# Kernel tuning notes

Hardware: AMD Instinct MI355X
Metric: run time of the kernel (lower is better)

Reference implementation:

```python
import jax, jax.numpy as jnp
import numpy as np

COMMITMENT_COST = 0.25
CODEBOOK_SIZE = 8192
EMBED_DIM = 256


def setup_inputs() -> dict:
    key = jax.random.key(0)
    k1, k2 = jax.random.split(key)
    z = jax.random.normal(k1, (16, 256, 32, 32), dtype=jnp.float32)
    # Embedding init: uniform(-1/K, 1/K)
    emb = jax.random.uniform(k2, (CODEBOOK_SIZE, EMBED_DIM), dtype=jnp.float32,
                             minval=-1.0 / CODEBOOK_SIZE, maxval=1.0 / CODEBOOK_SIZE)
    return {"z": z, "embedding": emb}


def reference(z, embedding):
    # z: [b, c, h, w] -> [b, h, w, c]
    z = jnp.transpose(z.astype(jnp.float32), (0, 2, 3, 1))
    b, h, w, c = z.shape
    zf = z.reshape(-1, c)  # [N, c]
    # Squared distances: ||z||^2 + ||e||^2 - 2 z e^T   -> [N, K]
    d = (jnp.sum(zf * zf, axis=1, keepdims=True)
         + jnp.sum(embedding * embedding, axis=1)
         - 2.0 * jnp.einsum('nd,kd->nk', zf, embedding))
    ids = jnp.argmin(d, axis=1)  # [N] int
    z_q = embedding[ids].reshape(b, h, w, c)
    commitment_loss = COMMITMENT_COST * jnp.mean((jax.lax.stop_gradient(z_q) - z) ** 2)
    codebook_loss = jnp.mean((z_q - jax.lax.stop_gradient(z)) ** 2)
    loss = commitment_loss + codebook_loss
    # straight-through estimator
    z_q_st = z + jax.lax.stop_gradient(z_q - z)
    z_q_out = jnp.transpose(z_q_st, (0, 3, 1, 2))  # [b, c, h, w]
    return (z_q_out, loss, commitment_loss, codebook_loss, ids)
```

## Files before the change

kernel.cpp:

```cpp
#include <hip/hip_runtime.h>

#define BB    16
#define CC    256
#define HWD   1024
#define NN    16384
#define KK    8192
#define DD    256
#define ZQ_N  4194304

#define WS_ROWBEST 0
#define WS_LOSS    131072
#define WS_NEEDED  131080

#define ZB_OFF      0
#define EB_OFF      2097152
#define Q_OFF       3145728
#define SEGCNT_OFF  4192256
#define BC_OFF      4194304
#define SEGCAP      8176u
#define LQCAP       3072

#define CMARGIN  4e-4f

typedef short short8 __attribute__((ext_vector_type(8)));
typedef float f32x4  __attribute__((ext_vector_type(4)));
typedef unsigned short u16;
typedef unsigned int   u32;

static __device__ __forceinline__ u32 cenc(float x) {
    u32 u = __float_as_uint(x);
    return (u & 0x80000000u) ? ~u : (u | 0x80000000u);
}
static __device__ __forceinline__ float cdec(u32 k) {
    u32 u = (k & 0x80000000u) ? (k ^ 0x80000000u) : ~k;
    return __uint_as_float(u);
}
static __device__ __forceinline__ u16 f2bf(float f) {
    u32 u = __float_as_uint(f);
    return (u16)((u + 0x7FFFu + ((u >> 16) & 1u)) >> 16);
}

__global__ __launch_bounds__(256)
void k_prep(const float* __restrict__ z, const float* __restrict__ emb,
            u16* __restrict__ zb, u16* __restrict__ eb,
            unsigned long long* __restrict__ rowBest, double* __restrict__ lossSum,
            u32* __restrict__ bestC, u32* __restrict__ segCnt) {
    __shared__ float tile[64][65];
    const int bid = blockIdx.x;
    const int t = threadIdx.x;
    if (bid < 1024) {
        const int b = bid >> 6, d0 = ((bid >> 4) & 3) * 64, h0 = (bid & 15) * 64;
        const float* zp = z + ((size_t)b * CC + d0) * HWD + h0;
#pragma unroll
        for (int i = 0; i < 4; ++i) {
            int fid = i * 256 + t;
            int dd = fid >> 4, hq = (fid & 15) * 4;
            float4 v = *(const float4*)(zp + (size_t)dd * HWD + hq);
            tile[dd][hq] = v.x; tile[dd][hq + 1] = v.y; tile[dd][hq + 2] = v.z; tile[dd][hq + 3] = v.w;
        }
        __syncthreads();
        u16* op = zb + ((size_t)b * HWD + h0) * DD + d0;
#pragma unroll
        for (int i = 0; i < 4; ++i) {
            int fid = i * 256 + t;
            int hh = fid >> 4, dq = (fid & 15) * 4;
            ushort4 o;
            o.x = f2bf(tile[dq + 0][hh]); o.y = f2bf(tile[dq + 1][hh]);
            o.z = f2bf(tile[dq + 2][hh]); o.w = f2bf(tile[dq + 3][hh]);
            *(ushort4*)(op + (size_t)hh * DD + dq) = o;
        }
    } else if (bid < 3072) {
        int i = (bid - 1024) * 256 + t;
        float4 v = ((const float4*)emb)[i];
        ushort4 o;
        o.x = f2bf(v.x); o.y = f2bf(v.y); o.z = f2bf(v.z); o.w = f2bf(v.w);
        ((ushort4*)eb)[i] = o;
    } else {
        int i = (bid - 3072) * 256 + t;
        if (i < NN) {
            rowBest[i] = (((unsigned long long)0xFF800000u) << 24) | 0xFFFFFFULL;
            bestC[i]   = 0xFFFFFFFFu;
        }
        if (i < 64) segCnt[i] = 0u;
        if (i == 64) *lossSum = 0.0;
    }
}

#define VMW4()  asm volatile("s_waitcnt vmcnt(4)"  ::: "memory")
#define VMW0()  asm volatile("s_waitcnt vmcnt(0)"  ::: "memory")
#define SBAR()  do { __builtin_amdgcn_s_barrier(); asm volatile("" ::: "memory"); } while (0)

__global__ __launch_bounds__(512, 2)
void k_gemm(const u16* __restrict__ zb, const u16* __restrict__ eb,
            u32* __restrict__ bestC, u32* __restrict__ segCnt, uint2* __restrict__ queue) {
    __shared__ __align__(16) char smem[98304];
    __shared__ u32 lqn, qbase;

    const int bid = blockIdx.x;
    const int xcd = bid & 7, idx = bid >> 3;
    const int bx = xcd * 8 + (idx & 7);
    const int by = idx >> 3;
    const int row0 = bx * 256, col0 = by * 256;

    const int t = threadIdx.x;
    const int wid = t >> 6, l = t & 63;
    const int wy = wid >> 1, wx = wid & 1;

    f32x4 acc[4][8];
#pragma unroll
    for (int mi = 0; mi < 4; ++mi)
#pragma unroll
        for (int ni = 0; ni < 8; ++ni) acc[mi][ni] = (f32x4){0.f, 0.f, 0.f, 0.f};

    const int rbase = wid * 32;
    const int srow   = l >> 2;
    const int schunk = (l & 3) ^ ((l >> 3) & 3);
    const int rchunk = (((l >> 4) ^ ((l >> 1) & 3)) << 4);
    const int rrow   = l & 15;

    auto stage = [&](int buf, int kc) {
        char* As = smem + buf * 32768;
        char* Bs = As + 16384;
#pragma unroll
        for (int j = 0; j < 2; ++j) {
            const int rl = rbase + j * 16 + srow;
            const u16* gA = zb + (size_t)(row0 + rl) * DD + kc + schunk * 8;
            __builtin_amdgcn_global_load_lds(
                (const __attribute__((address_space(1))) u32*)gA,
                (__attribute__((address_space(3))) u32*)(As + (rbase + j * 16) * 64), 16, 0, 0);
        }
#pragma unroll
        for (int j = 0; j < 2; ++j) {
            const int rl = rbase + j * 16 + srow;
            const u16* gB = eb + (size_t)(col0 + rl) * DD + kc + schunk * 8;
            __builtin_amdgcn_global_load_lds(
                (const __attribute__((address_space(1))) u32*)gB,
                (__attribute__((address_space(3))) u32*)(Bs + (rbase + j * 16) * 64), 16, 0, 0);
        }
    };

    auto compute = [&](int buf) {
        const char* As = smem + buf * 32768;
        const char* Bs = As + 16384;
        short8 a[4], b[8];
#pragma unroll
        for (int mi = 0; mi < 4; ++mi)
            a[mi] = *(const short8*)(As + (wy * 64 + mi * 16 + rrow) * 64 + rchunk);
#pragma unroll
        for (int ni = 0; ni < 8; ++ni)
            b[ni] = *(const short8*)(Bs + (wx * 128 + ni * 16 + rrow) * 64 + rchunk);
        __builtin_amdgcn_s_setprio(1);
#pragma unroll
        for (int mi = 0; mi < 4; ++mi)
#pragma unroll
            for (int ni = 0; ni < 8; ++ni)
                acc[mi][ni] = __builtin_amdgcn_mfma_f32_16x16x32_bf16(a[mi], b[ni], acc[mi][ni], 0, 0, 0);
        __builtin_amdgcn_s_setprio(0);
    };

    stage(0, 0); stage(1, 32);
    VMW4(); SBAR(); compute(0); stage(2, 64);
    VMW4(); SBAR(); compute(1); stage(0, 96);
    VMW4(); SBAR(); compute(2); stage(1, 128);
    VMW4(); SBAR(); compute(0); stage(2, 160);
    VMW4(); SBAR(); compute(1); stage(0, 192);
    VMW4(); SBAR(); compute(2); stage(1, 224);
    VMW4(); SBAR(); compute(0);
    VMW0(); SBAR(); compute(1);

    float* rm = (float*)(smem + 65536);
    u32* lqe  = (u32*)(smem + 65536 + 2048);
    u32* lqs  = lqe + LQCAP;

    float fmx[4][4];
#pragma unroll
    for (int mi = 0; mi < 4; ++mi)
#pragma unroll
        for (int r = 0; r < 4; ++r) {
            float v = fmaxf(fmaxf(acc[mi][0][r], acc[mi][1][r]), fmaxf(acc[mi][2][r], acc[mi][3][r]));
            v = fmaxf(v, fmaxf(fmaxf(acc[mi][4][r], acc[mi][5][r]), fmaxf(acc[mi][6][r], acc[mi][7][r])));
            fmx[mi][r] = v;
            v = fmaxf(v, __shfl_xor(v, 1));
            v = fmaxf(v, __shfl_xor(v, 2));
            v = fmaxf(v, __shfl_xor(v, 4));
            v = fmaxf(v, __shfl_xor(v, 8));
            if ((l & 15) == 0)
                rm[(wy * 64 + mi * 16 + ((l >> 4) << 2) + r) * 2 + wx] = -2.0f * v;
        }
    __syncthreads();

    if (t < 256) {
        float mn = fminf(rm[t * 2], rm[t * 2 + 1]);
        u32 old = atomicMin(bestC + row0 + t, cenc(mn));
        rm[t * 2] = fminf(mn, cdec(old));
    }
    if (t == 0) lqn = 0;
    __syncthreads();

    uint2* qseg = queue + (size_t)bx * SEGCAP;

#pragma unroll
    for (int mi = 0; mi < 4; ++mi)
#pragma unroll
        for (int r = 0; r < 4; ++r) {
            const int rl = wy * 64 + mi * 16 + ((l >> 4) << 2) + r;
            const float cut = rm[rl * 2] + CMARGIN;
            if (-2.0f * fmx[mi][r] > cut) continue;
            const int row = row0 + rl;
#pragma unroll
            for (int ni = 0; ni < 8; ++ni) {
                const float s = -2.0f * acc[mi][ni][r];
                if (s <= cut) {
                    const int col = col0 + wx * 128 + ni * 16 + (l & 15);
                    u32 li = atomicAdd(&lqn, 1u);
                    if (li < LQCAP) {
                        lqe[li] = ((u32)row << 13) | (u32)col;
                        lqs[li] = __float_as_uint(s);
                    } else {
                        u32 gi = atomicAdd(segCnt + bx, 1u);
                        if (gi < SEGCAP)
                            qseg[gi] = make_uint2(((u32)row << 13) | (u32)col, __float_as_uint(s));
                    }
                }
            }
        }
    __syncthreads();
    if (t == 0) {
        u32 n = min(lqn, (u32)LQCAP);
        lqn = n;
        qbase = atomicAdd(segCnt + bx, n);
    }
    __syncthreads();
    for (u32 i2 = t; i2 < lqn; i2 += 512) {
        u32 gi = qbase + i2;
        if (gi < SEGCAP) qseg[gi] = make_uint2(lqe[i2], lqs[i2]);
    }
}

__global__ __launch_bounds__(512)
void k_rescore(const float* __restrict__ z, const float* __restrict__ emb,
               const uint2* __restrict__ queue, const u32* __restrict__ segCnt,
               const u32* __restrict__ bestC,
               unsigned long long* __restrict__ rowBest) {
    __shared__ float zl[256][65];
    const int bid = blockIdx.x;
    const int seg  = bid >> 2;
    const int quar = bid & 3;
    const int b = seg >> 2;
    const int hwstart = ((seg & 3) << 8) + quar * 64;
    const int rlo = seg * 256 + quar * 64;

    const float* zsrc = z + (size_t)b * CC * HWD + hwstart;
    const int t = threadIdx.x;
#pragma unroll
    for (int i = 0; i < 32; ++i) {
        int idx = i * 512 + t;
        int d = idx >> 6, j = idx & 63;
        zl[d][j] = zsrc[(size_t)d * HWD + j];
    }
    __syncthreads();

    const u32 n = min(segCnt[seg], SEGCAP);
    const uint2* q = queue + (size_t)seg * SEGCAP;
    for (u32 i = t; i < n; i += 512) {
        const uint2 ent = q[i];
        const int row = (int)(ent.x >> 13);
        const u32 r = (u32)(row - rlo);
        if (r >= 64u) continue;
        const int col = (int)(ent.x & 8191u);
        const float s = __uint_as_float(ent.y);
        const float bound = cdec(bestC[row]);
        if (s > bound + CMARGIN) continue;

        const float* er = emb + (size_t)col * DD;

        float A0 = 0.f, A1 = 0.f, A2 = 0.f, A3 = 0.f;
        float zh0 = 0.f, eh0 = 0.f, z2 = 0.f, e2 = 0.f;
#pragma unroll
        for (int h = 0; h < 2; ++h) {
            const int base = h * 128;
            float zv[8], ev[8], rz[8], re[8];
#pragma unroll
            for (int q2 = 0; q2 < 8; ++q2) { zv[q2] = zl[base + q2][r]; ev[q2] = er[base + q2]; }
#pragma unroll
            for (int q2 = 0; q2 < 8; ++q2) { rz[q2] = __fmul_rn(zv[q2], zv[q2]); re[q2] = __fmul_rn(ev[q2], ev[q2]); }
            A0 = __fadd_rn(A0, __fmul_rn(zv[0], ev[0])); A1 = __fadd_rn(A1, __fmul_rn(zv[1], ev[1]));
            A2 = __fadd_rn(A2, __fmul_rn(zv[2], ev[2])); A3 = __fadd_rn(A3, __fmul_rn(zv[3], ev[3]));
            A0 = __fadd_rn(A0, __fmul_rn(zv[4], ev[4])); A1 = __fadd_rn(A1, __fmul_rn(zv[5], ev[5]));
            A2 = __fadd_rn(A2, __fmul_rn(zv[6], ev[6])); A3 = __fadd_rn(A3, __fmul_rn(zv[7], ev[7]));
            for (int i2 = 8; i2 < 128; i2 += 8) {
#pragma unroll
                for (int q2 = 0; q2 < 8; ++q2) { zv[q2] = zl[base + i2 + q2][r]; ev[q2] = er[base + i2 + q2]; }
#pragma unroll
                for (int q2 = 0; q2 < 8; ++q2) {
                    rz[q2] = __fadd_rn(rz[q2], __fmul_rn(zv[q2], zv[q2]));
                    re[q2] = __fadd_rn(re[q2], __fmul_rn(ev[q2], ev[q2]));
                }
                A0 = __fadd_rn(A0, __fmul_rn(zv[0], ev[0])); A1 = __fadd_rn(A1, __fmul_rn(zv[1], ev[1]));
                A2 = __fadd_rn(A2, __fmul_rn(zv[2], ev[2])); A3 = __fadd_rn(A3, __fmul_rn(zv[3], ev[3]));
                A0 = __fadd_rn(A0, __fmul_rn(zv[4], ev[4])); A1 = __fadd_rn(A1, __fmul_rn(zv[5], ev[5]));
                A2 = __fadd_rn(A2, __fmul_rn(zv[6], ev[6])); A3 = __fadd_rn(A3, __fmul_rn(zv[7], ev[7]));
            }
            float cz = __fadd_rn(__fadd_rn(__fadd_rn(rz[0], rz[1]), __fadd_rn(rz[2], rz[3])),
                                 __fadd_rn(__fadd_rn(rz[4], rz[5]), __fadd_rn(rz[6], rz[7])));
            float ce = __fadd_rn(__fadd_rn(__fadd_rn(re[0], re[1]), __fadd_rn(re[2], re[3])),
                                 __fadd_rn(__fadd_rn(re[4], re[5]), __fadd_rn(re[6], re[7])));
            if (h == 0) { zh0 = cz; eh0 = ce; }
            else        { z2 = __fadd_rn(zh0, cz); e2 = __fadd_rn(eh0, ce); }
        }
        const float dot = __fadd_rn(__fadd_rn(A0, A1), __fadd_rn(A2, A3));
        const float S   = __fadd_rn(z2, e2);
        const float d   = __fsub_rn(S, __fmul_rn(2.0f, dot));

        const u32 db = __float_as_uint(d);
        const u32 kd = (db & 0x80000000u) ? ~db : (db | 0x80000000u);
        const unsigned long long pk = (((unsigned long long)kd) << 24) | (unsigned long long)col;
        atomicMin(rowBest + row, pk);
    }
}

__global__ __launch_bounds__(256)
void k_gather(const float* __restrict__ z, const float* __restrict__ emb,
              const unsigned long long* __restrict__ rowBest,
              float* __restrict__ outZq, double* __restrict__ lossSum,
              float* __restrict__ outIds) {
    __shared__ float lt[128][65];
    __shared__ u32 idr[128];
    __shared__ double red[4];
    const int t = threadIdx.x;
    const int hw0 = blockIdx.x * 128, b = blockIdx.y;
    const int h2 = blockIdx.z;
    const int w = t >> 6, l = t & 63;

    if (t < 128) {
        u32 id = (u32)(rowBest[b * HWD + hw0 + t] & 0xFFFFFFULL) & (KK - 1);
        idr[t] = id;
        if (h2 == 0) outIds[b * HWD + hw0 + t] = (float)id;
    }
    __syncthreads();

    const int rr = t >> 6, cc = t & 63;
    for (int s = 0; s < 32; ++s) {
        const int r = s * 4 + rr;
        lt[r][cc] = emb[(size_t)idr[r] * DD + h2 * 64 + cc];
    }
    __syncthreads();

    double lsum = 0.0;
#pragma unroll
    for (int i = 0; i < 16; ++i) {
        const int cl = i * 4 + w;
        const int c  = h2 * 64 + cl;
        const size_t f = ((size_t)(b * CC + c)) * HWD + hw0 + 2 * l;
        const float2 zv = *(const float2*)(z + f);
        float2 zq;
        zq.x = lt[2 * l][cl];
        zq.y = lt[2 * l + 1][cl];
        *(float2*)(outZq + f) = zq;
        const double d0 = (double)zq.x - (double)zv.x;
        const double d1 = (double)zq.y - (double)zv.y;
        lsum += d0 * d0 + d1 * d1;
    }
#pragma unroll
    for (int o = 32; o; o >>= 1) lsum += __shfl_down(lsum, o);
    if (l == 0) red[w] = lsum;
    __syncthreads();
    if (t == 0) atomicAdd(lossSum, red[0] + red[1] + red[2] + red[3]);
}

__global__ void k_loss(const double* __restrict__ lossSum, float* __restrict__ outLoss) {
    double m = *lossSum / (double)ZQ_N;
    outLoss[0] = (float)(1.25 * m);
    outLoss[1] = (float)(0.25 * m);
    outLoss[2] = (float)m;
}

extern "C" void kernel_launch(void* const* d_in, const int* in_sizes, int n_in,
                              void* d_out, int out_size, void* d_ws, size_t ws_size,
                              hipStream_t stream) {
    const float* z   = (const float*)d_in[0];
    const float* emb = (const float*)d_in[1];
    float* out = (float*)d_out;
    char* ws = (char*)d_ws;

    if (ws_size < (size_t)WS_NEEDED) return;

    unsigned long long* rowBest = (unsigned long long*)(ws + WS_ROWBEST);
    double*             lossSum = (double*)(ws + WS_LOSS);
    u16*   zb     = (u16*)(out + ZB_OFF);
    u16*   eb     = (u16*)(out + EB_OFF);
    uint2* queue  = (uint2*)(out + Q_OFF);
    u32*   segCnt = (u32*)(out + SEGCNT_OFF);
    u32*   bestC  = (u32*)(out + BC_OFF);

    hipLaunchKernelGGL(k_prep,    dim3(3136),        dim3(256), 0, stream,
                       z, emb, zb, eb, rowBest, lossSum, bestC, segCnt);
    hipLaunchKernelGGL(k_gemm,    dim3(2048),        dim3(512), 0, stream, zb, eb, bestC, segCnt, queue);
    hipLaunchKernelGGL(k_rescore, dim3(256),         dim3(512), 0, stream, z, emb, queue, segCnt, bestC, rowBest);
    hipLaunchKernelGGL(k_gather,  dim3(8, 16, 4),    dim3(256), 0, stream,
                       z, emb, rowBest, out, lossSum, out + ZQ_N + 3);
    hipLaunchKernelGGL(k_loss,    dim3(1),           dim3(1),   0, stream, lossSum, out + ZQ_N);
}
```

Measured before the change: 178.2 us.

## Split candidate queue per 128-row half so rescore blocks scan fewer entries

The candidate queue is now split into two segments per 256-row GEMM tile, one per 128-row half, each with its own local LDS queue and global counter. Rescore blocks map to a segment half and 64-row slice, so each block scans only entries from its half instead of the whole 256-row segment, where most entries were skipped. Per-segment capacity is halved, which raises the risk of overflowing and dropping candidates when they cluster in one half.

```diff
diff --git a/kernel.cpp b/kernel.cpp
--- a/kernel.cpp
+++ b/kernel.cpp
@@ -17,8 +17,8 @@
 #define Q_OFF       3145728
 #define SEGCNT_OFF  4192256
 #define BC_OFF      4194304
-#define SEGCAP      8176u
-#define LQCAP       3072
+#define SEGCAP      4088u
+#define LQCAP       1536
 
 #define CMARGIN  4e-4f
 
@@ -81,8 +81,8 @@
             rowBest[i] = (((unsigned long long)0xFF800000u) << 24) | 0xFFFFFFULL;
             bestC[i]   = 0xFFFFFFFFu;
         }
-        if (i < 64) segCnt[i] = 0u;
-        if (i == 64) *lossSum = 0.0;
+        if (i < 128) segCnt[i] = 0u;
+        if (i == 128) *lossSum = 0.0;
     }
 }
 
@@ -94,7 +94,7 @@
 void k_gemm(const u16* __restrict__ zb, const u16* __restrict__ eb,
             u32* __restrict__ bestC, u32* __restrict__ segCnt, uint2* __restrict__ queue) {
     __shared__ __align__(16) char smem[98304];
-    __shared__ u32 lqn, qbase;
+    __shared__ u32 lqn0, lqn1, qb0, qb1;
 
     const int bid = blockIdx.x;
     const int xcd = bid & 7, idx = bid >> 3;
@@ -169,8 +169,10 @@
     VMW0(); SBAR(); compute(1);
 
     float* rm = (float*)(smem + 65536);
-    u32* lqe  = (u32*)(smem + 65536 + 2048);
-    u32* lqs  = lqe + LQCAP;
+    u32* lqe0 = (u32*)(smem + 65536 + 2048);
+    u32* lqs0 = lqe0 + LQCAP;
+    u32* lqe1 = lqs0 + LQCAP;
+    u32* lqs1 = lqe1 + LQCAP;
 
     float fmx[4][4];
 #pragma unroll
@@ -194,46 +196,65 @@
         u32 old = atomicMin(bestC + row0 + t, cenc(mn));
         rm[t * 2] = fminf(mn, cdec(old));
     }
-    if (t == 0) lqn = 0;
-    __syncthreads();
-
-    uint2* qseg = queue + (size_t)bx * SEGCAP;
-
-#pragma unroll
-    for (int mi = 0; mi < 4; ++mi)
-#pragma unroll
-        for (int r = 0; r < 4; ++r) {
-            const int rl = wy * 64 + mi * 16 + ((l >> 4) << 2) + r;
-            const float cut = rm[rl * 2] + CMARGIN;
-            if (-2.0f * fmx[mi][r] > cut) continue;
-            const int row = row0 + rl;
-#pragma unroll
-            for (int ni = 0; ni < 8; ++ni) {
-                const float s = -2.0f * acc[mi][ni][r];
-                if (s <= cut) {
-                    const int col = col0 + wx * 128 + ni * 16 + (l & 15);
-                    u32 li = atomicAdd(&lqn, 1u);
-                    if (li < LQCAP) {
-                        lqe[li] = ((u32)row << 13) | (u32)col;
-                        lqs[li] = __float_as_uint(s);
-                    } else {
-                        u32 gi = atomicAdd(segCnt + bx, 1u);
-                        if (gi < SEGCAP)
-                            qseg[gi] = make_uint2(((u32)row << 13) | (u32)col, __float_as_uint(s));
+    if (t == 0) { lqn0 = 0; lqn1 = 0; }
+    __syncthreads();
+
+    {
+        const int half = wy >> 1;
+        u32* lqe = half ? lqe1 : lqe0;
+        u32* lqs = half ? lqs1 : lqs0;
+        u32* lqnp = half ? &lqn1 : &lqn0;
+        uint2* qseg = queue + (size_t)(bx * 2 + half) * SEGCAP;
+        u32* scp = segCnt + bx * 2 + half;
+#pragma unroll
+        for (int mi = 0; mi < 4; ++mi)
+#pragma unroll
+            for (int r = 0; r < 4; ++r) {
+                const int rl = wy * 64 + mi * 16 + ((l >> 4) << 2) + r;
+                const float cut = rm[rl * 2] + CMARGIN;
+                if (-2.0f * fmx[mi][r] > cut) continue;
+                const int row = row0 + rl;
+#pragma unroll
+                for (int ni = 0; ni < 8; ++ni) {
+                    const float s = -2.0f * acc[mi][ni][r];
+                    if (s <= cut) {
+                        const int col = col0 + wx * 128 + ni * 16 + (l & 15);
+                        u32 li = atomicAdd(lqnp, 1u);
+                        if (li < LQCAP) {
+                            lqe[li] = ((u32)row << 13) | (u32)col;
+                            lqs[li] = __float_as_uint(s);
+                        } else {
+                            u32 gi = atomicAdd(scp, 1u);
+                            if (gi < SEGCAP)
+                                qseg[gi] = make_uint2(((u32)row << 13) | (u32)col, __float_as_uint(s));
+                        }
                     }
                 }
             }
-        }
+    }
     __syncthreads();
     if (t == 0) {
-        u32 n = min(lqn, (u32)LQCAP);
-        lqn = n;
-        qbase = atomicAdd(segCnt + bx, n);
-    }
-    __syncthreads();
-    for (u32 i2 = t; i2 < lqn; i2 += 512) {
-        u32 gi = qbase + i2;
-        if (gi < SEGCAP) qseg[gi] = make_uint2(lqe[i2], lqs[i2]);
+        u32 n = min(lqn0, (u32)LQCAP);
+        lqn0 = n;
+        qb0 = atomicAdd(segCnt + bx * 2, n);
+    }
+    if (t == 1) {
+        u32 n = min(lqn1, (u32)LQCAP);
+        lqn1 = n;
+        qb1 = atomicAdd(segCnt + bx * 2 + 1, n);
+    }
+    __syncthreads();
+    {
+        uint2* qs0 = queue + (size_t)(bx * 2) * SEGCAP;
+        for (u32 i2 = t; i2 < lqn0; i2 += 512) {
+            u32 gi = qb0 + i2;
+            if (gi < SEGCAP) qs0[gi] = make_uint2(lqe0[i2], lqs0[i2]);
+        }
+        uint2* qs1 = queue + (size_t)(bx * 2 + 1) * SEGCAP;
+        for (u32 i2 = t; i2 < lqn1; i2 += 512) {
+            u32 gi = qb1 + i2;
+            if (gi < SEGCAP) qs1[gi] = make_uint2(lqe1[i2], lqs1[i2]);
+        }
     }
 }
 
@@ -244,11 +265,11 @@
                unsigned long long* __restrict__ rowBest) {
     __shared__ float zl[256][65];
     const int bid = blockIdx.x;
-    const int seg  = bid >> 2;
-    const int quar = bid & 3;
-    const int b = seg >> 2;
-    const int hwstart = ((seg & 3) << 8) + quar * 64;
-    const int rlo = seg * 256 + quar * 64;
+    const int seg  = bid >> 1;
+    const int half = bid & 1;
+    const int b = seg >> 3;
+    const int hwstart = ((seg & 7) << 7) + half * 64;
+    const int rlo = seg * 128 + half * 64;
 
     const float* zsrc = z + (size_t)b * CC * HWD + hwstart;
     const int t = threadIdx.x;
```

After: 167.8 us. 1.06x faster.
